# Optimization experiments

Hardware: AMD Instinct MI355X
Metric: run time of the kernel (lower is better)

Reference implementation:

```python
import jax, jax.numpy as jnp
import numpy as np

B, S, D = 2, 2048, 1024
H, KVH, HD = 16, 4, 64
WINDOW = 64
N_REP = H // KVH
ROPE_THETA = 10000.0


def _rope(x, cos, sin):
    # x: (b, s, h, hd); treat last dim as interleaved (real, imag) pairs
    xr = x.reshape(*x.shape[:-1], HD // 2, 2)
    a, b = xr[..., 0], xr[..., 1]
    c = cos[None, :, None, :]  # (1, s, 1, hd/2)
    s_ = sin[None, :, None, :]
    out = jnp.stack([a * c - b * s_, a * s_ + b * c], axis=-1)
    return out.reshape(x.shape)


def setup_inputs() -> dict:
    key = jax.random.key(0)
    ks = jax.random.split(key, 5)
    x = jax.random.normal(ks[0], (B, S, D), dtype=jnp.float32)
    # rope frequencies (deterministic, as in Mistral/LLaMA)
    inv_freq = 1.0 / (ROPE_THETA ** (np.arange(0, HD, 2, dtype=np.float32) / HD))
    t = np.arange(S, dtype=np.float32)
    freqs = np.outer(t, inv_freq)  # (S, HD/2)
    freqs_cos = jnp.asarray(np.cos(freqs), dtype=jnp.float32)
    freqs_sin = jnp.asarray(np.sin(freqs), dtype=jnp.float32)
    sc = 0.02
    wq = jax.random.normal(ks[1], (D, H * HD), dtype=jnp.float32) * sc
    wk = jax.random.normal(ks[2], (D, KVH * HD), dtype=jnp.float32) * sc
    wv = jax.random.normal(ks[3], (D, KVH * HD), dtype=jnp.float32) * sc
    wo = jax.random.normal(ks[4], (H * HD, D), dtype=jnp.float32) * sc
    return {"x": x, "freqs_cos": freqs_cos, "freqs_sin": freqs_sin,
            "wq": wq, "wk": wk, "wv": wv, "wo": wo}


def reference(x, freqs_cos, freqs_sin, wq, wk, wv, wo):
    b, s, _ = x.shape
    q = (x @ wq).reshape(b, s, H, HD)
    k = (x @ wk).reshape(b, s, KVH, HD)
    v = (x @ wv).reshape(b, s, KVH, HD)
    q = _rope(q, freqs_cos, freqs_sin)
    k = _rope(k, freqs_cos, freqs_sin)
    # repeat_kv (GQA): expand kv heads by n_rep, kv-head-major ordering
    k = jnp.repeat(k, N_REP, axis=2)  # (b, s, H, hd)
    v = jnp.repeat(v, N_REP, axis=2)
    scores = jnp.einsum('bihd,bjhd->bhij', q, k) / jnp.sqrt(jnp.float32(HD))
    pos = jnp.arange(s)
    dist = pos[None, :] - pos[:, None]  # dist[i,j] = j - i
    banned = (dist > 0) | (dist < -WINDOW)  # causal + sliding window of 64
    mask = jnp.where(banned, jnp.float32(-jnp.inf), jnp.float32(0.0))
    scores = scores + mask[None, None, :, :]
    scores = jnp.maximum(scores, -1e9)  # clamp(min=-1e9)
    attn = jax.nn.softmax(scores.astype(jnp.float32), axis=-1).astype(q.dtype)
    out = jnp.einsum('bhij,bjhd->bihd', attn, v).reshape(b, s, H * HD)
    return out @ wo
```

## Files before the change

### kernel.cpp

```cpp
#include <hip/hip_runtime.h>
#include <hip/hip_bf16.h>

constexpr int B = 2, S = 2048, D = 1024;
constexpr int H = 16, KVH = 4, HD = 64;
constexpr int BS = B * S;
constexpr int QS = 1536;

typedef __attribute__((ext_vector_type(8))) short short8;
typedef __attribute__((ext_vector_type(4))) float floatx4;

#define GPTR(p) ((__attribute__((address_space(1))) void*)(p))
#define LPTR(p) ((__attribute__((address_space(3))) void*)(p))

static __device__ __forceinline__ unsigned short f2bf(float f) {
  union { float f; unsigned u; } c{f};
  unsigned r = (c.u + 0x7FFFu + ((c.u >> 16) & 1u)) >> 16;
  return (unsigned short)r;
}

__global__ __launch_bounds__(256) void prep_kernel(
    const float* __restrict__ x,
    const float* __restrict__ wq, const float* __restrict__ wk,
    const float* __restrict__ wv, const float* __restrict__ wo,
    unsigned short* __restrict__ xb,
    unsigned short* __restrict__ wqkvT, unsigned short* __restrict__ woT) {
  int bz = blockIdx.x;
  if (bz < 4096) {
    int t = bz * 256 + threadIdx.x;
    float4 v = ((const float4*)x)[t];
    ushort4 o;
    o.x = f2bf(v.x); o.y = f2bf(v.y); o.z = f2bf(v.z); o.w = f2bf(v.w);
    ((ushort4*)xb)[t] = o;
    return;
  }
  __shared__ float t[32][33];
  int z = bz - 4096;
  int zx = z % 80, zy = z / 80;
  const float* src; unsigned short* dst; int N, dstOff, nb;
  if (zx < 32)      { src = wq; dst = wqkvT; N = 1024; dstOff = 0;    nb = zx; }
  else if (zx < 40) { src = wk; dst = wqkvT; N = 256;  dstOff = 1024; nb = zx - 32; }
  else if (zx < 48) { src = wv; dst = wqkvT; N = 256;  dstOff = 1280; nb = zx - 40; }
  else              { src = wo; dst = woT;   N = 1024; dstOff = 0;    nb = zx - 48; }
  int n0 = nb * 32, k0 = zy * 32;
  int tx = threadIdx.x & 31, ty = threadIdx.x >> 5;
#pragma unroll
  for (int r = 0; r < 4; ++r)
    t[ty + r * 8][tx] = src[(size_t)(k0 + ty + r * 8) * N + n0 + tx];
  __syncthreads();
#pragma unroll
  for (int r = 0; r < 4; ++r)
    dst[(size_t)(dstOff + n0 + ty + r * 8) * D + k0 + tx] = f2bf(t[tx][ty + r * 8]);
}

__global__ __launch_bounds__(256) void gemm_qkv_kernel(
    const unsigned short* __restrict__ A, const unsigned short* __restrict__ Bt,
    const float* __restrict__ cs, const float* __restrict__ sn,
    unsigned short* __restrict__ qb, unsigned short* __restrict__ kb,
    unsigned short* __restrict__ vt) {
  constexpr int K = 1024;
  __shared__ unsigned short As[128 * 32];
  __shared__ unsigned short Bs[128 * 32];
  const int tid = threadIdx.x;
  const int lane = tid & 63, wvid = tid >> 6;
  const int wy = wvid >> 1, wx = wvid & 1;
  const int quad = lane >> 4, lrow = lane & 15;
  const size_t row0 = (size_t)blockIdx.y * 128;
  const size_t col0 = (size_t)blockIdx.x * 128;

  floatx4 acc[4][4];
#pragma unroll
  for (int i = 0; i < 4; ++i)
#pragma unroll
    for (int j = 0; j < 4; ++j) acc[i][j] = floatx4{0.f, 0.f, 0.f, 0.f};

  const int srow = wvid * 32 + (lane >> 2);
  const int schk = (lane & 3) * 8;
  const unsigned short* ga0 = A  + (row0 + srow) * K + schk;
  const unsigned short* ga1 = ga0 + 16 * K;
  const unsigned short* gb0 = Bt + (col0 + srow) * K + schk;
  const unsigned short* gb1 = gb0 + 16 * K;
  char* ldsA = (char*)As + wvid * 2048;
  char* ldsB = (char*)Bs + wvid * 2048;

  for (int k0 = 0; k0 < K; k0 += 32) {
    __syncthreads();
    __builtin_amdgcn_global_load_lds(GPTR(ga0 + k0), LPTR(ldsA), 16, 0, 0);
    __builtin_amdgcn_global_load_lds(GPTR(ga1 + k0), LPTR(ldsA + 1024), 16, 0, 0);
    __builtin_amdgcn_global_load_lds(GPTR(gb0 + k0), LPTR(ldsB), 16, 0, 0);
    __builtin_amdgcn_global_load_lds(GPTR(gb1 + k0), LPTR(ldsB + 1024), 16, 0, 0);
    __syncthreads();

    short8 af[4], bg[4];
#pragma unroll
    for (int mi = 0; mi < 4; ++mi)
      af[mi] = *(const short8*)&As[(wy * 64 + mi * 16 + lrow) * 32 + quad * 8];
#pragma unroll
    for (int ni = 0; ni < 4; ++ni)
      bg[ni] = *(const short8*)&Bs[(wx * 64 + ni * 16 + lrow) * 32 + quad * 8];
#pragma unroll
    for (int mi = 0; mi < 4; ++mi)
#pragma unroll
      for (int ni = 0; ni < 4; ++ni)
        acc[mi][ni] = __builtin_amdgcn_mfma_f32_16x16x32_bf16(af[mi], bg[ni], acc[mi][ni], 0, 0, 0);
  }

  const int col_wave = (int)col0 + wx * 64;
  const int h = col_wave >> 6;
  const int sb = (int)(row0 & 2047) + wy * 64;
  const int bidx = (int)(row0 >> 11);

  if (h < 20) {
    unsigned short* dst = (h < 16) ? qb : kb;
    const int dstride = (h < 16) ? 1024 : 256;
    const int dcol = (h < 16) ? (col_wave + 0) : (col_wave - 1024);
    const int f = (lrow + 0) >> 1;
    const bool ev = (lrow & 1) == 0;
#pragma unroll
    for (int mi = 0; mi < 4; ++mi) {
#pragma unroll
      for (int ni = 0; ni < 4; ++ni) {
        int ff = (ni * 16 + lrow) >> 1;
#pragma unroll
        for (int r = 0; r < 4; ++r) {
          int s = sb + mi * 16 + quad * 4 + r;
          float v = acc[mi][ni][r];
          float p = __shfl_xor(v, 1);
          float c = cs[s * 32 + ff];
          float si = sn[s * 32 + ff];
          float o = ev ? (v * c - p * si) : (v * c + p * si);
          size_t row = row0 + wy * 64 + mi * 16 + quad * 4 + r;
          dst[row * dstride + dcol + ni * 16 + lrow] = f2bf(o);
        }
      }
    }
    (void)f;
  } else {
    const int kvh = h - 20;
    const int g = bidx * KVH + kvh;
#pragma unroll
    for (int mi = 0; mi < 4; ++mi) {
#pragma unroll
      for (int ni = 0; ni < 4; ++ni) {
        int d = ni * 16 + lrow;
        int s0 = sb + mi * 16 + quad * 4;
        ushort4 o;
        o.x = f2bf(acc[mi][ni][0]); o.y = f2bf(acc[mi][ni][1]);
        o.z = f2bf(acc[mi][ni][2]); o.w = f2bf(acc[mi][ni][3]);
        *(ushort4*)&vt[((size_t)(g * 64 + d)) * S + s0] = o;
      }
    }
  }
}

__global__ __launch_bounds__(256) void gemm_bt_kernel(
    const unsigned short* __restrict__ A, const unsigned short* __restrict__ Bt,
    float* __restrict__ C, int N, int K) {
  __shared__ unsigned short As[128 * 32];
  __shared__ unsigned short Bs[128 * 32];
  const int tid = threadIdx.x;
  const int lane = tid & 63, wvid = tid >> 6;
  const int wy = wvid >> 1, wx = wvid & 1;
  const int quad = lane >> 4, lrow = lane & 15;
  const size_t row0 = (size_t)blockIdx.y * 128;
  const size_t col0 = (size_t)blockIdx.x * 128;

  floatx4 acc[4][4];
#pragma unroll
  for (int i = 0; i < 4; ++i)
#pragma unroll
    for (int j = 0; j < 4; ++j) acc[i][j] = floatx4{0.f, 0.f, 0.f, 0.f};

  const int srow = wvid * 32 + (lane >> 2);
  const int schk = (lane & 3) * 8;
  const unsigned short* ga0 = A  + (row0 + srow) * K + schk;
  const unsigned short* ga1 = ga0 + 16 * K;
  const unsigned short* gb0 = Bt + (col0 + srow) * K + schk;
  const unsigned short* gb1 = gb0 + 16 * K;
  char* ldsA = (char*)As + wvid * 2048;
  char* ldsB = (char*)Bs + wvid * 2048;

  for (int k0 = 0; k0 < K; k0 += 32) {
    __syncthreads();
    __builtin_amdgcn_global_load_lds(GPTR(ga0 + k0), LPTR(ldsA), 16, 0, 0);
    __builtin_amdgcn_global_load_lds(GPTR(ga1 + k0), LPTR(ldsA + 1024), 16, 0, 0);
    __builtin_amdgcn_global_load_lds(GPTR(gb0 + k0), LPTR(ldsB), 16, 0, 0);
    __builtin_amdgcn_global_load_lds(GPTR(gb1 + k0), LPTR(ldsB + 1024), 16, 0, 0);
    __syncthreads();

    short8 af[4], bg[4];
#pragma unroll
    for (int mi = 0; mi < 4; ++mi)
      af[mi] = *(const short8*)&As[(wy * 64 + mi * 16 + lrow) * 32 + quad * 8];
#pragma unroll
    for (int ni = 0; ni < 4; ++ni)
      bg[ni] = *(const short8*)&Bs[(wx * 64 + ni * 16 + lrow) * 32 + quad * 8];
#pragma unroll
    for (int mi = 0; mi < 4; ++mi)
#pragma unroll
      for (int ni = 0; ni < 4; ++ni)
        acc[mi][ni] = __builtin_amdgcn_mfma_f32_16x16x32_bf16(af[mi], bg[ni], acc[mi][ni], 0, 0, 0);
  }

#pragma unroll
  for (int mi = 0; mi < 4; ++mi)
#pragma unroll
    for (int ni = 0; ni < 4; ++ni) {
      size_t col = col0 + wx * 64 + ni * 16 + lrow;
      size_t rowb = row0 + wy * 64 + mi * 16 + quad * 4;
#pragma unroll
      for (int r = 0; r < 4; ++r)
        C[(rowb + r) * N + col] = acc[mi][ni][r];
    }
}

__global__ __launch_bounds__(256) void attn_kernel(
    const unsigned short* __restrict__ qb,
    const unsigned short* __restrict__ kb,
    const unsigned short* __restrict__ vt,
    unsigned short* __restrict__ ao) {
  __shared__ __align__(16) unsigned short plds[4][16][104];
  const int w = threadIdx.x >> 6, lane = threadIdx.x & 63;
  const int lrow = lane & 15, quad = lane >> 4;
  const int wg = blockIdx.x * 4 + w;
  const int h = wg & (H - 1);
  const int qblk = wg >> 4;
  const int i0 = (qblk & (S / 16 - 1)) * 16;
  const int b = qblk >> 7;
  const int kvh = h >> 2;
  const int jbase = i0 - 80;

  const unsigned short* qrow = qb + (size_t)(b * S + i0 + lrow) * 1024 + h * 64 + quad * 8;
  short8 qf0 = *(const short8*)qrow;
  short8 qf1 = *(const short8*)(qrow + 32);

  floatx4 sc[6];
#pragma unroll
  for (int t = 0; t < 6; ++t) {
    int j = jbase + t * 16 + lrow;
    int jc = j < 0 ? 0 : j;
    const unsigned short* krow = kb + (size_t)(b * S + jc) * 256 + kvh * 64 + quad * 8;
    short8 kf0 = *(const short8*)krow;
    short8 kf1 = *(const short8*)(krow + 32);
    floatx4 a = {0.f, 0.f, 0.f, 0.f};
    a = __builtin_amdgcn_mfma_f32_16x16x32_bf16(qf0, kf0, a, 0, 0, 0);
    a = __builtin_amdgcn_mfma_f32_16x16x32_bf16(qf1, kf1, a, 0, 0, 0);
    sc[t] = a;
  }

  float sv[6][4];
  float mx[4] = {-1e30f, -1e30f, -1e30f, -1e30f};
#pragma unroll
  for (int t = 0; t < 6; ++t) {
    int j = jbase + t * 16 + lrow;
#pragma unroll
    for (int r = 0; r < 4; ++r) {
      int dji = (i0 + quad * 4 + r) - j;
      bool valid = (j >= 0) && (dji >= 0) && (dji <= 64);
      float s = valid ? sc[t][r] * 0.125f : -1e30f;
      sv[t][r] = s;
      mx[r] = fmaxf(mx[r], s);
    }
  }
#pragma unroll
  for (int r = 0; r < 4; ++r)
#pragma unroll
    for (int off = 8; off > 0; off >>= 1)
      mx[r] = fmaxf(mx[r], __shfl_xor(mx[r], off));

  float ls[4] = {0.f, 0.f, 0.f, 0.f};
#pragma unroll
  for (int t = 0; t < 6; ++t)
#pragma unroll
    for (int r = 0; r < 4; ++r) {
      float e = __expf(sv[t][r] - mx[r]);
      sv[t][r] = e;
      ls[r] += e;
    }
#pragma unroll
  for (int r = 0; r < 4; ++r) {
#pragma unroll
    for (int off = 8; off > 0; off >>= 1)
      ls[r] += __shfl_xor(ls[r], off);
    ls[r] = 1.f / ls[r];
  }
#pragma unroll
  for (int t = 0; t < 6; ++t)
#pragma unroll
    for (int r = 0; r < 4; ++r)
      plds[w][quad * 4 + r][t * 16 + lrow] = f2bf(sv[t][r] * ls[r]);
  __syncthreads();

  floatx4 oc[4];
#pragma unroll
  for (int mt = 0; mt < 4; ++mt) oc[mt] = floatx4{0.f, 0.f, 0.f, 0.f};
  const unsigned short* vbase = vt + (size_t)(b * KVH + kvh) * 64 * S;
#pragma unroll
  for (int c = 0; c < 3; ++c) {
    short8 pf = *(const short8*)&plds[w][lrow][c * 32 + quad * 8];
    int j = jbase + c * 32 + quad * 8;
    int jc = j < 0 ? 0 : j;
#pragma unroll
    for (int mt = 0; mt < 4; ++mt) {
      short8 vf = *(const short8*)(vbase + (size_t)(mt * 16 + lrow) * S + jc);
      oc[mt] = __builtin_amdgcn_mfma_f32_16x16x32_bf16(vf, pf, oc[mt], 0, 0, 0);
    }
  }

#pragma unroll
  for (int mt = 0; mt < 4; ++mt) {
    ushort4 o;
    o.x = f2bf(oc[mt][0]); o.y = f2bf(oc[mt][1]);
    o.z = f2bf(oc[mt][2]); o.w = f2bf(oc[mt][3]);
    *(ushort4*)(ao + (size_t)(b * S + i0 + lrow) * 1024 + h * 64 + mt * 16 + quad * 4) = o;
  }
}

extern "C" void kernel_launch(void* const* d_in, const int* in_sizes, int n_in,
                              void* d_out, int out_size, void* d_ws, size_t ws_size,
                              hipStream_t stream) {
  const float* x  = (const float*)d_in[0];
  const float* fc = (const float*)d_in[1];
  const float* fs = (const float*)d_in[2];
  const float* wq = (const float*)d_in[3];
  const float* wk = (const float*)d_in[4];
  const float* wv = (const float*)d_in[5];
  const float* wo = (const float*)d_in[6];
  float* out = (float*)d_out;

  char* base = (char*)d_ws;
  unsigned short* xb    = (unsigned short*)base;
  unsigned short* wqkvT = (unsigned short*)(base + (8u << 20));
  unsigned short* woT   = (unsigned short*)(base + (11u << 20));
  unsigned short* qb    = (unsigned short*)(base + (13u << 20));
  unsigned short* kb    = (unsigned short*)(base + (21u << 20));
  unsigned short* vT    = (unsigned short*)(base + (23u << 20));
  unsigned short* ao    = (unsigned short*)(base + (25u << 20));

  prep_kernel<<<4096 + 2560, 256, 0, stream>>>(x, wq, wk, wv, wo, xb, wqkvT, woT);

  gemm_qkv_kernel<<<dim3(QS / 128, BS / 128), 256, 0, stream>>>(
      xb, wqkvT, fc, fs, qb, kb, vT);

  attn_kernel<<<(BS / 16) * H / 4, 256, 0, stream>>>(qb, kb, vT, ao);

  gemm_bt_kernel<<<dim3(D / 128, BS / 128), 256, 0, stream>>>(ao, woT, out, D, D);
}
```

Baseline: 154.7 us.

## Fuse fp32-to-bf16 conversion and weight transpose into GEMM operand loading

Removes the separate prep kernel that converted x to bf16 and transposed and converted the weights. Both GEMMs now read fp32 x and weights directly, convert them to bf16 in registers and write them transposed into LDS. Tiles become 128x64 with a K step of 64 split into two sub-stages, and the grid is reordered so the row index varies fastest, which doubles the block count. This saves a kernel launch and a round trip of intermediate buffers, but it re-reads and re-converts fp32 operands in every block, doubling their global traffic, and replaces the async global-to-LDS loads with synchronous register staging.

```diff
diff --git a/kernel.cpp b/kernel.cpp
--- a/kernel.cpp
+++ b/kernel.cpp
@@ -17,109 +17,120 @@
   unsigned r = (c.u + 0x7FFFu + ((c.u >> 16) & 1u)) >> 16;
   return (unsigned short)r;
 }
-
-__global__ __launch_bounds__(256) void prep_kernel(
+static __device__ __forceinline__ short8 pack8(float4 a, float4 b) {
+  short8 r;
+  r[0] = (short)f2bf(a.x); r[1] = (short)f2bf(a.y);
+  r[2] = (short)f2bf(a.z); r[3] = (short)f2bf(a.w);
+  r[4] = (short)f2bf(b.x); r[5] = (short)f2bf(b.y);
+  r[6] = (short)f2bf(b.z); r[7] = (short)f2bf(b.w);
+  return r;
+}
+
+__global__ __launch_bounds__(256) void gemm_qkv_kernel(
     const float* __restrict__ x,
     const float* __restrict__ wq, const float* __restrict__ wk,
-    const float* __restrict__ wv, const float* __restrict__ wo,
-    unsigned short* __restrict__ xb,
-    unsigned short* __restrict__ wqkvT, unsigned short* __restrict__ woT) {
-  int bz = blockIdx.x;
-  if (bz < 4096) {
-    int t = bz * 256 + threadIdx.x;
-    float4 v = ((const float4*)x)[t];
-    ushort4 o;
-    o.x = f2bf(v.x); o.y = f2bf(v.y); o.z = f2bf(v.z); o.w = f2bf(v.w);
-    ((ushort4*)xb)[t] = o;
-    return;
-  }
-  __shared__ float t[32][33];
-  int z = bz - 4096;
-  int zx = z % 80, zy = z / 80;
-  const float* src; unsigned short* dst; int N, dstOff, nb;
-  if (zx < 32)      { src = wq; dst = wqkvT; N = 1024; dstOff = 0;    nb = zx; }
-  else if (zx < 40) { src = wk; dst = wqkvT; N = 256;  dstOff = 1024; nb = zx - 32; }
-  else if (zx < 48) { src = wv; dst = wqkvT; N = 256;  dstOff = 1280; nb = zx - 40; }
-  else              { src = wo; dst = woT;   N = 1024; dstOff = 0;    nb = zx - 48; }
-  int n0 = nb * 32, k0 = zy * 32;
-  int tx = threadIdx.x & 31, ty = threadIdx.x >> 5;
-#pragma unroll
-  for (int r = 0; r < 4; ++r)
-    t[ty + r * 8][tx] = src[(size_t)(k0 + ty + r * 8) * N + n0 + tx];
-  __syncthreads();
-#pragma unroll
-  for (int r = 0; r < 4; ++r)
-    dst[(size_t)(dstOff + n0 + ty + r * 8) * D + k0 + tx] = f2bf(t[tx][ty + r * 8]);
-}
-
-__global__ __launch_bounds__(256) void gemm_qkv_kernel(
-    const unsigned short* __restrict__ A, const unsigned short* __restrict__ Bt,
+    const float* __restrict__ wv,
     const float* __restrict__ cs, const float* __restrict__ sn,
     unsigned short* __restrict__ qb, unsigned short* __restrict__ kb,
     unsigned short* __restrict__ vt) {
-  constexpr int K = 1024;
-  __shared__ unsigned short As[128 * 32];
-  __shared__ unsigned short Bs[128 * 32];
+  __shared__ unsigned short As[2 * 128 * 32];
+  __shared__ unsigned short Bs[2 * 64 * 32];
   const int tid = threadIdx.x;
   const int lane = tid & 63, wvid = tid >> 6;
   const int wy = wvid >> 1, wx = wvid & 1;
   const int quad = lane >> 4, lrow = lane & 15;
-  const size_t row0 = (size_t)blockIdx.y * 128;
-  const size_t col0 = (size_t)blockIdx.x * 128;
-
-  floatx4 acc[4][4];
+  const size_t row0 = (size_t)blockIdx.x * 128;
+  const size_t col0 = (size_t)blockIdx.y * 64;
+
+  const float* wsrc; int Nw, cb;
+  if (col0 < 1024)      { wsrc = wq; Nw = 1024; cb = (int)col0; }
+  else if (col0 < 1280) { wsrc = wk; Nw = 256;  cb = (int)col0 - 1024; }
+  else                  { wsrc = wv; Nw = 256;  cb = (int)col0 - 1280; }
+
+  floatx4 acc[4][2];
 #pragma unroll
   for (int i = 0; i < 4; ++i)
 #pragma unroll
-    for (int j = 0; j < 4; ++j) acc[i][j] = floatx4{0.f, 0.f, 0.f, 0.f};
-
-  const int srow = wvid * 32 + (lane >> 2);
-  const int schk = (lane & 3) * 8;
-  const unsigned short* ga0 = A  + (row0 + srow) * K + schk;
-  const unsigned short* ga1 = ga0 + 16 * K;
-  const unsigned short* gb0 = Bt + (col0 + srow) * K + schk;
-  const unsigned short* gb1 = gb0 + 16 * K;
-  char* ldsA = (char*)As + wvid * 2048;
-  char* ldsB = (char*)Bs + wvid * 2048;
-
-  for (int k0 = 0; k0 < K; k0 += 32) {
+    for (int j = 0; j < 2; ++j) acc[i][j] = floatx4{0.f, 0.f, 0.f, 0.f};
+
+  const int ar = tid >> 2;
+  const int akc = (tid & 3) * 8;
+  const float* gxa = x + (row0 + ar) * 1024 + akc;
+  const float* gxb = x + (row0 + 64 + ar) * 1024 + akc;
+  const int aoff = ar * 32 + akc;
+
+  const int bsec = tid >> 7;
+  const int bu = tid & 127;
+  const int bn = (bu & 15) * 4;
+  const int bk = (bu >> 4) * 4;
+  const float* gw = wsrc + (size_t)(bsec * 32 + bk) * Nw + cb + bn;
+
+  for (int k0 = 0; k0 < 1024; k0 += 64) {
+    float4 al0 = *(const float4*)(gxa + k0);
+    float4 al1 = *(const float4*)(gxa + k0 + 4);
+    float4 al2 = *(const float4*)(gxa + k0 + 32);
+    float4 al3 = *(const float4*)(gxa + k0 + 36);
+    float4 ah0 = *(const float4*)(gxb + k0);
+    float4 ah1 = *(const float4*)(gxb + k0 + 4);
+    float4 ah2 = *(const float4*)(gxb + k0 + 32);
+    float4 ah3 = *(const float4*)(gxb + k0 + 36);
+    const float* gwk = gw + (size_t)k0 * Nw;
+    float4 b0 = *(const float4*)(gwk);
+    float4 b1 = *(const float4*)(gwk + Nw);
+    float4 b2 = *(const float4*)(gwk + 2 * Nw);
+    float4 b3 = *(const float4*)(gwk + 3 * Nw);
+
     __syncthreads();
-    __builtin_amdgcn_global_load_lds(GPTR(ga0 + k0), LPTR(ldsA), 16, 0, 0);
-    __builtin_amdgcn_global_load_lds(GPTR(ga1 + k0), LPTR(ldsA + 1024), 16, 0, 0);
-    __builtin_amdgcn_global_load_lds(GPTR(gb0 + k0), LPTR(ldsB), 16, 0, 0);
-    __builtin_amdgcn_global_load_lds(GPTR(gb1 + k0), LPTR(ldsB + 1024), 16, 0, 0);
+    *(short8*)&As[aoff]               = pack8(al0, al1);
+    *(short8*)&As[2048 + aoff]        = pack8(ah0, ah1);
+    *(short8*)&As[4096 + aoff]        = pack8(al2, al3);
+    *(short8*)&As[4096 + 2048 + aoff] = pack8(ah2, ah3);
+#pragma unroll
+    for (int dn = 0; dn < 4; ++dn) {
+      const float* c0 = (const float*)&b0;
+      const float* c1 = (const float*)&b1;
+      const float* c2 = (const float*)&b2;
+      const float* c3 = (const float*)&b3;
+      uint2 o;
+      o.x = (unsigned)f2bf(c0[dn]) | ((unsigned)f2bf(c1[dn]) << 16);
+      o.y = (unsigned)f2bf(c2[dn]) | ((unsigned)f2bf(c3[dn]) << 16);
+      *(uint2*)&Bs[bsec * 2048 + (bn + dn) * 32 + bk] = o;
+    }
     __syncthreads();
 
-    short8 af[4], bg[4];
-#pragma unroll
-    for (int mi = 0; mi < 4; ++mi)
-      af[mi] = *(const short8*)&As[(wy * 64 + mi * 16 + lrow) * 32 + quad * 8];
-#pragma unroll
-    for (int ni = 0; ni < 4; ++ni)
-      bg[ni] = *(const short8*)&Bs[(wx * 64 + ni * 16 + lrow) * 32 + quad * 8];
-#pragma unroll
-    for (int mi = 0; mi < 4; ++mi)
-#pragma unroll
-      for (int ni = 0; ni < 4; ++ni)
-        acc[mi][ni] = __builtin_amdgcn_mfma_f32_16x16x32_bf16(af[mi], bg[ni], acc[mi][ni], 0, 0, 0);
-  }
-
-  const int col_wave = (int)col0 + wx * 64;
+#pragma unroll
+    for (int s = 0; s < 2; ++s) {
+      short8 af[4], bg[2];
+#pragma unroll
+      for (int mi = 0; mi < 4; ++mi)
+        af[mi] = *(const short8*)&As[s * 4096 + (wy * 64 + mi * 16 + lrow) * 32 + quad * 8];
+#pragma unroll
+      for (int ni = 0; ni < 2; ++ni)
+        bg[ni] = *(const short8*)&Bs[s * 2048 + (wx * 32 + ni * 16 + lrow) * 32 + quad * 8];
+#pragma unroll
+      for (int mi = 0; mi < 4; ++mi)
+#pragma unroll
+        for (int ni = 0; ni < 2; ++ni)
+          acc[mi][ni] = __builtin_amdgcn_mfma_f32_16x16x32_bf16(af[mi], bg[ni], acc[mi][ni], 0, 0, 0);
+    }
+  }
+
+  const int col_wave = (int)col0 + wx * 32;
   const int h = col_wave >> 6;
+  const int hc = col_wave & 63;
   const int sb = (int)(row0 & 2047) + wy * 64;
   const int bidx = (int)(row0 >> 11);
 
   if (h < 20) {
     unsigned short* dst = (h < 16) ? qb : kb;
     const int dstride = (h < 16) ? 1024 : 256;
-    const int dcol = (h < 16) ? (col_wave + 0) : (col_wave - 1024);
-    const int f = (lrow + 0) >> 1;
+    const int dcol = (h < 16) ? col_wave : (col_wave - 1024);
     const bool ev = (lrow & 1) == 0;
 #pragma unroll
     for (int mi = 0; mi < 4; ++mi) {
 #pragma unroll
-      for (int ni = 0; ni < 4; ++ni) {
-        int ff = (ni * 16 + lrow) >> 1;
+      for (int ni = 0; ni < 2; ++ni) {
+        int ff = (hc + ni * 16 + lrow) >> 1;
 #pragma unroll
         for (int r = 0; r < 4; ++r) {
           int s = sb + mi * 16 + quad * 4 + r;
@@ -133,15 +144,14 @@
         }
       }
     }
-    (void)f;
   } else {
     const int kvh = h - 20;
     const int g = bidx * KVH + kvh;
 #pragma unroll
     for (int mi = 0; mi < 4; ++mi) {
 #pragma unroll
-      for (int ni = 0; ni < 4; ++ni) {
-        int d = ni * 16 + lrow;
+      for (int ni = 0; ni < 2; ++ni) {
+        int d = hc + ni * 16 + lrow;
         int s0 = sb + mi * 16 + quad * 4;
         ushort4 o;
         o.x = f2bf(acc[mi][ni][0]); o.y = f2bf(acc[mi][ni][1]);
@@ -153,63 +163,88 @@
 }
 
 __global__ __launch_bounds__(256) void gemm_bt_kernel(
-    const unsigned short* __restrict__ A, const unsigned short* __restrict__ Bt,
-    float* __restrict__ C, int N, int K) {
-  __shared__ unsigned short As[128 * 32];
-  __shared__ unsigned short Bs[128 * 32];
+    const unsigned short* __restrict__ ao, const float* __restrict__ wo,
+    float* __restrict__ out) {
+  __shared__ unsigned short As[2 * 128 * 32];
+  __shared__ unsigned short Bs[2 * 64 * 32];
   const int tid = threadIdx.x;
   const int lane = tid & 63, wvid = tid >> 6;
   const int wy = wvid >> 1, wx = wvid & 1;
   const int quad = lane >> 4, lrow = lane & 15;
-  const size_t row0 = (size_t)blockIdx.y * 128;
-  const size_t col0 = (size_t)blockIdx.x * 128;
-
-  floatx4 acc[4][4];
+  const size_t row0 = (size_t)blockIdx.x * 128;
+  const size_t col0 = (size_t)blockIdx.y * 64;
+
+  floatx4 acc[4][2];
 #pragma unroll
   for (int i = 0; i < 4; ++i)
 #pragma unroll
-    for (int j = 0; j < 4; ++j) acc[i][j] = floatx4{0.f, 0.f, 0.f, 0.f};
+    for (int j = 0; j < 2; ++j) acc[i][j] = floatx4{0.f, 0.f, 0.f, 0.f};
 
   const int srow = wvid * 32 + (lane >> 2);
   const int schk = (lane & 3) * 8;
-  const unsigned short* ga0 = A  + (row0 + srow) * K + schk;
-  const unsigned short* ga1 = ga0 + 16 * K;
-  const unsigned short* gb0 = Bt + (col0 + srow) * K + schk;
-  const unsigned short* gb1 = gb0 + 16 * K;
+  const unsigned short* gA = ao + (row0 + srow) * 1024 + schk;
   char* ldsA = (char*)As + wvid * 2048;
-  char* ldsB = (char*)Bs + wvid * 2048;
-
-  for (int k0 = 0; k0 < K; k0 += 32) {
+
+  const int bsec = tid >> 7;
+  const int bu = tid & 127;
+  const int bn = (bu & 15) * 4;
+  const int bk = (bu >> 4) * 4;
+  const float* gw = wo + (size_t)(bsec * 32 + bk) * 1024 + col0 + bn;
+
+  for (int k0 = 0; k0 < 1024; k0 += 64) {
+    const float* gwk = gw + (size_t)k0 * 1024;
+    float4 b0 = *(const float4*)(gwk);
+    float4 b1 = *(const float4*)(gwk + 1024);
+    float4 b2 = *(const float4*)(gwk + 2048);
+    float4 b3 = *(const float4*)(gwk + 3072);
+
     __syncthreads();
-    __builtin_amdgcn_global_load_lds(GPTR(ga0 + k0), LPTR(ldsA), 16, 0, 0);
-    __builtin_amdgcn_global_load_lds(GPTR(ga1 + k0), LPTR(ldsA + 1024), 16, 0, 0);
-    __builtin_amdgcn_global_load_lds(GPTR(gb0 + k0), LPTR(ldsB), 16, 0, 0);
-    __builtin_amdgcn_global_load_lds(GPTR(gb1 + k0), LPTR(ldsB + 1024), 16, 0, 0);
+#pragma unroll
+    for (int s = 0; s < 2; ++s) {
+      __builtin_amdgcn_global_load_lds(GPTR(gA + k0 + s * 32),
+                                       LPTR(ldsA + s * 8192), 16, 0, 0);
+      __builtin_amdgcn_global_load_lds(GPTR(gA + 16 * 1024 + k0 + s * 32),
+                                       LPTR(ldsA + s * 8192 + 1024), 16, 0, 0);
+    }
+#pragma unroll
+    for (int dn = 0; dn < 4; ++dn) {
+      const float* c0 = (const float*)&b0;
+      const float* c1 = (const float*)&b1;
+      const float* c2 = (const float*)&b2;
+      const float* c3 = (const float*)&b3;
+      uint2 o;
+      o.x = (unsigned)f2bf(c0[dn]) | ((unsigned)f2bf(c1[dn]) << 16);
+      o.y = (unsigned)f2bf(c2[dn]) | ((unsigned)f2bf(c3[dn]) << 16);
+      *(uint2*)&Bs[bsec * 2048 + (bn + dn) * 32 + bk] = o;
+    }
     __syncthreads();
 
-    short8 af[4], bg[4];
-#pragma unroll
-    for (int mi = 0; mi < 4; ++mi)
-      af[mi] = *(const short8*)&As[(wy * 64 + mi * 16 + lrow) * 32 + quad * 8];
-#pragma unroll
-    for (int ni = 0; ni < 4; ++ni)
-      bg[ni] = *(const short8*)&Bs[(wx * 64 + ni * 16 + lrow) * 32 + quad * 8];
-#pragma unroll
-    for (int mi = 0; mi < 4; ++mi)
-#pragma unroll
-      for (int ni = 0; ni < 4; ++ni)
-        acc[mi][ni] = __builtin_amdgcn_mfma_f32_16x16x32_bf16(af[mi], bg[ni], acc[mi][ni], 0, 0, 0);
+#pragma unroll
+    for (int s = 0; s < 2; ++s) {
+      short8 af[4], bg[2];
+#pragma unroll
+      for (int mi = 0; mi < 4; ++mi)
+        af[mi] = *(const short8*)&As[s * 4096 + (wy * 64 + mi * 16 + lrow) * 32 + quad * 8];
+#pragma unroll
+      for (int ni = 0; ni < 2; ++ni)
+        bg[ni] = *(const short8*)&Bs[s * 2048 + (wx * 32 + ni * 16 + lrow) * 32 + quad * 8];
+#pragma unroll
+      for (int mi = 0; mi < 4; ++mi)
+#pragma unroll
+        for (int ni = 0; ni < 2; ++ni)
+          acc[mi][ni] = __builtin_amdgcn_mfma_f32_16x16x32_bf16(af[mi], bg[ni], acc[mi][ni], 0, 0, 0);
+    }
   }
 
 #pragma unroll
   for (int mi = 0; mi < 4; ++mi)
 #pragma unroll
-    for (int ni = 0; ni < 4; ++ni) {
-      size_t col = col0 + wx * 64 + ni * 16 + lrow;
+    for (int ni = 0; ni < 2; ++ni) {
+      size_t col = col0 + wx * 32 + ni * 16 + lrow;
       size_t rowb = row0 + wy * 64 + mi * 16 + quad * 4;
 #pragma unroll
       for (int r = 0; r < 4; ++r)
-        C[(rowb + r) * N + col] = acc[mi][ni][r];
+        out[(rowb + r) * 1024 + col] = acc[mi][ni][r];
     }
 }
 
@@ -328,20 +363,15 @@
   float* out = (float*)d_out;
 
   char* base = (char*)d_ws;
-  unsigned short* xb    = (unsigned short*)base;
-  unsigned short* wqkvT = (unsigned short*)(base + (8u << 20));
-  unsigned short* woT   = (unsigned short*)(base + (11u << 20));
-  unsigned short* qb    = (unsigned short*)(base + (13u << 20));
-  unsigned short* kb    = (unsigned short*)(base + (21u << 20));
-  unsigned short* vT    = (unsigned short*)(base + (23u << 20));
-  unsigned short* ao    = (unsigned short*)(base + (25u << 20));
-
-  prep_kernel<<<4096 + 2560, 256, 0, stream>>>(x, wq, wk, wv, wo, xb, wqkvT, woT);
-
-  gemm_qkv_kernel<<<dim3(QS / 128, BS / 128), 256, 0, stream>>>(
-      xb, wqkvT, fc, fs, qb, kb, vT);
+  unsigned short* qb = (unsigned short*)base;
+  unsigned short* kb = (unsigned short*)(base + (8u << 20));
+  unsigned short* vT = (unsigned short*)(base + (10u << 20));
+  unsigned short* ao = (unsigned short*)(base + (12u << 20));
+
+  gemm_qkv_kernel<<<dim3(BS / 128, QS / 64), 256, 0, stream>>>(
+      x, wq, wk, wv, fc, fs, qb, kb, vT);
 
   attn_kernel<<<(BS / 16) * H / 4, 256, 0, stream>>>(qb, kb, vT, ao);
 
-  gemm_bt_kernel<<<dim3(D / 128, BS / 128), 256, 0, stream>>>(ao, woT, out, D, D);
-}
+  gemm_bt_kernel<<<dim3(BS / 128, D / 64), 256, 0, stream>>>(ao, wo, out);
+}
```

Result: slower. 179.6 us (+16.1%).
